# Kernel optimization log

Hardware: AMD Instinct MI355X
Metric: run time of the kernel (lower is better)

## Reference

```python
import jax, jax.numpy as jnp
import numpy as np

LAMBDA = 0.01  # sparsity_threshold
SCALE = 0.02
NUM_BLOCKS = 4


def setup_inputs() -> dict:
    key = jax.random.key(0)
    k1, k2, k3, k4, k5 = jax.random.split(key, 5)
    B, N, C = 8, 4096, 512
    bs = C // NUM_BLOCKS
    return {
        "x": jax.random.normal(k1, (B, N, C), dtype=jnp.float32),
        "w1": jax.random.normal(k2, (2, NUM_BLOCKS, bs, bs), dtype=jnp.float32) * SCALE,
        "w2": jax.random.normal(k3, (2, NUM_BLOCKS, bs, bs), dtype=jnp.float32) * SCALE,
        "b1": jax.random.normal(k4, (2, NUM_BLOCKS, bs), dtype=jnp.float32) * SCALE,
        "b2": jax.random.normal(k5, (2, NUM_BLOCKS, bs), dtype=jnp.float32) * SCALE,
        "H": 64,
        "W": 64,
    }


def _softshrink(v):
    return jnp.where(v > LAMBDA, v - LAMBDA, jnp.where(v < -LAMBDA, v + LAMBDA, jnp.zeros((), v.dtype)))


def reference(x, w1, w2, b1, b2, H, W):
    B, N, C = x.shape
    bs = C // NUM_BLOCKS
    xb = x.reshape(B, N, NUM_BLOCKS, bs)
    # FFT over (token, block) axes, ortho norm — faithful to torch fft2(dim=(1,2))
    xf = jnp.fft.fft2(xb, axes=(1, 2), norm="ortho")
    re, im = jnp.real(xf), jnp.imag(xf)

    mul = lambda a, w: jnp.einsum("tnbd,bdk->tnbk", a, w)  # block-diagonal matmul

    r1 = jax.nn.relu(mul(re, w1[0]) - mul(im, w1[1]) + b1[0])
    i1 = jax.nn.relu(mul(re, w1[1]) + mul(im, w1[0]) + b1[1])
    r2 = mul(r1, w2[0]) - mul(i1, w2[1]) + b2[0]
    i2 = mul(r1, w2[1]) + mul(i1, w2[0]) + b2[1]

    z = _softshrink(r2) + 1j * _softshrink(i2)
    out = jnp.real(jnp.fft.ifft2(z, axes=(1, 2), norm="ortho"))  # .to(float32) keeps real part
    return out.reshape(B, N, C).astype(jnp.float32)
```

## Files before the change

### kernel.cpp

```cpp
#include <hip/hip_runtime.h>
#include <math.h>

#define TWO_PI 6.283185307179586f

typedef __attribute__((ext_vector_type(8))) short bf16x8;
typedef __attribute__((ext_vector_type(4))) short bf16x4;
typedef __attribute__((ext_vector_type(4))) float f32x4;
typedef __attribute__((ext_vector_type(4))) _Float16 h16x4;
typedef __attribute__((ext_vector_type(8))) _Float16 h16x8;

__device__ __forceinline__ short f2bf(float f) {
    unsigned u = __float_as_uint(f);
    unsigned r = (u + 0x7FFFu + ((u >> 16) & 1u)) >> 16;
    return (short)r;
}
__device__ __forceinline__ float bf2f(short s) {
    return __uint_as_float(((unsigned)(unsigned short)s) << 16);
}

__device__ __forceinline__ int dr4(int s) {
    return ((s & 3) << 4) | (s & 12) | ((s >> 4) & 3);
}

__device__ __forceinline__ void cmulw(float& xr, float& xi, float wr, float wi) {
    const float tr = xr * wr - xi * wi;
    xi = xr * wi + xi * wr;
    xr = tr;
}

template<int W>
__device__ __forceinline__ void fft64_dif4v(_Float16 (*Lre)[W], _Float16 (*Lim)[W],
                                            const float* wtr, const float* wti,
                                            int c4, int h) {
#pragma unroll
    for (int s = 0; s < 3; ++s) {
        const int q  = 16 >> (2 * s);
        const int tw = 1 << (2 * s);
        __syncthreads();
        const int j = h & (q - 1);
        const int g = (s == 0) ? 0 : (h >> (4 - 2 * s));
        const int i0 = g * (q << 2) + j;
        const int i1 = i0 + q, i2 = i1 + q, i3 = i2 + q;
        const h16x4 A0r = *(const h16x4*)&Lre[i0][c4], A0i = *(const h16x4*)&Lim[i0][c4];
        const h16x4 A1r = *(const h16x4*)&Lre[i1][c4], A1i = *(const h16x4*)&Lim[i1][c4];
        const h16x4 A2r = *(const h16x4*)&Lre[i2][c4], A2i = *(const h16x4*)&Lim[i2][c4];
        const h16x4 A3r = *(const h16x4*)&Lre[i3][c4], A3i = *(const h16x4*)&Lim[i3][c4];
        const int m = j * tw;
        const float w1r = wtr[m],     w1i = wti[m];
        const float w2r = wtr[2 * m], w2i = wti[2 * m];
        const float w3r = wtr[3 * m], w3i = wti[3 * m];
        h16x4 O0r, O0i, O1r, O1i, O2r, O2i, O3r, O3i;
#pragma unroll
        for (int e = 0; e < 4; ++e) {
            const float a0r = (float)A0r[e], a0i = (float)A0i[e];
            const float a1r = (float)A1r[e], a1i = (float)A1i[e];
            const float a2r = (float)A2r[e], a2i = (float)A2i[e];
            const float a3r = (float)A3r[e], a3i = (float)A3i[e];
            const float t0r = a0r + a2r, t0i = a0i + a2i;
            const float t2r = a0r - a2r, t2i = a0i - a2i;
            const float t1r = a1r + a3r, t1i = a1i + a3i;
            const float dr  = a1r - a3r, di  = a1i - a3i;
            const float t3r = di, t3i = -dr;
            O0r[e] = (_Float16)(t0r + t1r);  O0i[e] = (_Float16)(t0i + t1i);
            float y1r = t2r + t3r, y1i = t2i + t3i;
            float y2r = t0r - t1r, y2i = t0i - t1i;
            float y3r = t2r - t3r, y3i = t2i - t3i;
            if (m) {
                cmulw(y1r, y1i, w1r, w1i);
                cmulw(y2r, y2i, w2r, w2i);
                cmulw(y3r, y3i, w3r, w3i);
            }
            O1r[e] = (_Float16)y1r; O1i[e] = (_Float16)y1i;
            O2r[e] = (_Float16)y2r; O2i[e] = (_Float16)y2i;
            O3r[e] = (_Float16)y3r; O3i[e] = (_Float16)y3i;
        }
        *(h16x4*)&Lre[i0][c4] = O0r;  *(h16x4*)&Lim[i0][c4] = O0i;
        *(h16x4*)&Lre[i1][c4] = O1r;  *(h16x4*)&Lim[i1][c4] = O1i;
        *(h16x4*)&Lre[i2][c4] = O2r;  *(h16x4*)&Lim[i2][c4] = O2i;
        *(h16x4*)&Lre[i3][c4] = O3r;  *(h16x4*)&Lim[i3][c4] = O3i;
    }
    __syncthreads();
}

template<int W>
__device__ __forceinline__ void fft64_dit4v(_Float16 (*Lre)[W], _Float16 (*Lim)[W],
                                            const float* wtr, const float* wti,
                                            int c4, int h) {
#pragma unroll
    for (int s = 2; s >= 0; --s) {
        const int q  = 16 >> (2 * s);
        const int tw = 1 << (2 * s);
        __syncthreads();
        const int j = h & (q - 1);
        const int g = (s == 0) ? 0 : (h >> (4 - 2 * s));
        const int i0 = g * (q << 2) + j;
        const int i1 = i0 + q, i2 = i1 + q, i3 = i2 + q;
        const h16x4 A0r = *(const h16x4*)&Lre[i0][c4], A0i = *(const h16x4*)&Lim[i0][c4];
        const h16x4 A1r = *(const h16x4*)&Lre[i1][c4], A1i = *(const h16x4*)&Lim[i1][c4];
        const h16x4 A2r = *(const h16x4*)&Lre[i2][c4], A2i = *(const h16x4*)&Lim[i2][c4];
        const h16x4 A3r = *(const h16x4*)&Lre[i3][c4], A3i = *(const h16x4*)&Lim[i3][c4];
        const int m = j * tw;
        const float w1r = wtr[m],     w1i = -wti[m];
        const float w2r = wtr[2 * m], w2i = -wti[2 * m];
        const float w3r = wtr[3 * m], w3i = -wti[3 * m];
        h16x4 O0r, O0i, O1r, O1i, O2r, O2i, O3r, O3i;
#pragma unroll
        for (int e = 0; e < 4; ++e) {
            float b1r = (float)A1r[e], b1i = (float)A1i[e];
            float b2r = (float)A2r[e], b2i = (float)A2i[e];
            float b3r = (float)A3r[e], b3i = (float)A3i[e];
            if (m) {
                cmulw(b1r, b1i, w1r, w1i);
                cmulw(b2r, b2i, w2r, w2i);
                cmulw(b3r, b3i, w3r, w3i);
            }
            const float a0r = (float)A0r[e], a0i = (float)A0i[e];
            const float u0r = a0r + b2r, u0i = a0i + b2i;
            const float u1r = a0r - b2r, u1i = a0i - b2i;
            const float u2r = b1r + b3r, u2i = b1i + b3i;
            const float dr  = b1r - b3r, di  = b1i - b3i;
            const float u3r = -di, u3i = dr;
            O0r[e] = (_Float16)(u0r + u2r); O0i[e] = (_Float16)(u0i + u2i);
            O1r[e] = (_Float16)(u1r + u3r); O1i[e] = (_Float16)(u1i + u3i);
            O2r[e] = (_Float16)(u0r - u2r); O2i[e] = (_Float16)(u0i - u2i);
            O3r[e] = (_Float16)(u1r - u3r); O3i[e] = (_Float16)(u1i - u3i);
        }
        *(h16x4*)&Lre[i0][c4] = O0r;  *(h16x4*)&Lim[i0][c4] = O0i;
        *(h16x4*)&Lre[i1][c4] = O1r;  *(h16x4*)&Lim[i1][c4] = O1i;
        *(h16x4*)&Lre[i2][c4] = O2r;  *(h16x4*)&Lim[i2][c4] = O2i;
        *(h16x4*)&Lre[i3][c4] = O3r;  *(h16x4*)&Lim[i3][c4] = O3i;
    }
    __syncthreads();
}

#define DECODE_BCT() \
    const int b  = blockIdx.x >> 8; \
    const int dg = (blockIdx.x >> 2) & 63; \
    const int ct = blockIdx.x & 3;

#define GADDR(slot, blk, f4) \
    (((size_t)(b * 4096 + (slot)) * 512) + (size_t)((blk) * 128 + ct * 32 + (f4) * 4))

#define GADDR8(slot, blk, e8) \
    (((size_t)(b * 4096 + (slot)) * 512) + (size_t)((blk) * 128 + ct * 32 + (e8) * 8))

#define SETUP_TABLE48() \
    if (tid < 48) { \
        float s_, c_; \
        sincosf(TWO_PI * (float)tid / 64.0f, &s_, &c_); \
        wre[tid] = c_; wim[tid] = -s_; \
    }

extern "C" __global__ void __launch_bounds__(512)
fft_fwd_a(const float* __restrict__ x, short* __restrict__ zre, short* __restrict__ zim) {
    __shared__ __align__(16) _Float16 Lre[64][136];
    __shared__ __align__(16) _Float16 Lim[64][136];
    __shared__ float wre[48], wim[48];
    __shared__ float twr[64], twi[64];
    const int tid = threadIdx.x;
    SETUP_TABLE48();
    DECODE_BCT();
    if (tid >= 64 && tid < 128) {
        const int s1 = tid - 64;
        float sn, cs;
        sincosf(-(TWO_PI / 4096.0f) * (float)(dg * dr4(s1)), &sn, &cs);
        twr[s1] = cs; twi[s1] = sn;
    }
    for (int idx = tid; idx < 2048; idx += 512) {
        const int n1 = idx >> 5, q = idx & 31, blk = q >> 3, f4 = q & 7;
        const int cl = blk * 32 + f4 * 4;
        const float4 v = *(const float4*)(x + GADDR(n1 * 64 + dg, blk, f4));
        h16x4 hv, hz;
        hv[0] = (_Float16)v.x; hv[1] = (_Float16)v.y;
        hv[2] = (_Float16)v.z; hv[3] = (_Float16)v.w;
        hz[0] = (_Float16)0.f; hz[1] = (_Float16)0.f;
        hz[2] = (_Float16)0.f; hz[3] = (_Float16)0.f;
        *(h16x4*)&Lre[n1][cl] = hv;
        *(h16x4*)&Lim[n1][cl] = hz;
    }
    fft64_dif4v<136>(Lre, Lim, wre, wim, (tid & 31) * 4, tid >> 5);
    {
        const int s1 = tid >> 3, f4 = tid & 7;
        const float cs = twr[s1], sn = twi[s1];
        f32x4 r[4], m[4];
#pragma unroll
        for (int blk = 0; blk < 4; ++blk) {
            const int cl = blk * 32 + f4 * 4;
            const h16x4 hr = *(const h16x4*)&Lre[s1][cl];
            const h16x4 hi = *(const h16x4*)&Lim[s1][cl];
#pragma unroll
            for (int e = 0; e < 4; ++e) {
                const float vr = (float)hr[e], vi = (float)hi[e];
                r[blk][e] = vr * cs - vi * sn;
                m[blk][e] = vr * sn + vi * cs;
            }
        }
        const float sc = 1.0f / 128.0f;
        f32x4 yr[4], ym[4];
#pragma unroll
        for (int e = 0; e < 4; ++e) {
            const float r0 = r[0][e], r1 = r[1][e], r2 = r[2][e], r3 = r[3][e];
            const float m0 = m[0][e], m1 = m[1][e], m2 = m[2][e], m3 = m[3][e];
            yr[0][e] = (r0 + r1 + r2 + r3) * sc;  ym[0][e] = (m0 + m1 + m2 + m3) * sc;
            yr[1][e] = (r0 + m1 - r2 - m3) * sc;  ym[1][e] = (m0 - r1 - m2 + r3) * sc;
            yr[2][e] = (r0 - r1 + r2 - r3) * sc;  ym[2][e] = (m0 - m1 + m2 - m3) * sc;
            yr[3][e] = (r0 - m1 - r2 + m3) * sc;  ym[3][e] = (m0 + r1 - m2 - r3) * sc;
        }
#pragma unroll
        for (int blk = 0; blk < 4; ++blk) {
            bf16x4 pr, pi;
#pragma unroll
            for (int e = 0; e < 4; ++e) {
                pr[e] = f2bf(yr[blk][e]);
                pi[e] = f2bf(ym[blk][e]);
            }
            const size_t g = GADDR(s1 * 64 + dg, blk, f4);
            *(bf16x4*)(zre + g) = pr;
            *(bf16x4*)(zim + g) = pi;
        }
    }
}

extern "C" __global__ void __launch_bounds__(512)
fft_fwd_b(short* __restrict__ zre, short* __restrict__ zim) {
    __shared__ __align__(16) _Float16 Lre[64][136];
    __shared__ __align__(16) _Float16 Lim[64][136];
    __shared__ float wre[48], wim[48];
    const int tid = threadIdx.x;
    SETUP_TABLE48();
    DECODE_BCT();
    for (int idx = tid; idx < 1024; idx += 512) {
        const int n2 = idx >> 4, q = idx & 15, blk = q >> 2, e8 = q & 3;
        const int cl = blk * 32 + e8 * 8;
        const size_t g = GADDR8(dg * 64 + n2, blk, e8);
        const bf16x8 vr = *(const bf16x8*)(zre + g);
        const bf16x8 vi = *(const bf16x8*)(zim + g);
        h16x8 hr, hi;
#pragma unroll
        for (int i = 0; i < 8; ++i) {
            hr[i] = (_Float16)bf2f(vr[i]);
            hi[i] = (_Float16)bf2f(vi[i]);
        }
        *(h16x8*)&Lre[n2][cl] = hr;
        *(h16x8*)&Lim[n2][cl] = hi;
    }
    fft64_dif4v<136>(Lre, Lim, wre, wim, (tid & 31) * 4, tid >> 5);
    for (int idx = tid; idx < 1024; idx += 512) {
        const int s2 = idx >> 4, q = idx & 15, blk = q >> 2, e8 = q & 3;
        const int cl = blk * 32 + e8 * 8;
        const h16x8 hr = *(const h16x8*)&Lre[s2][cl];
        const h16x8 hi = *(const h16x8*)&Lim[s2][cl];
        bf16x8 pr, pi;
#pragma unroll
        for (int i = 0; i < 8; ++i) {
            pr[i] = f2bf((float)hr[i]);
            pi[i] = f2bf((float)hi[i]);
        }
        const size_t g = GADDR8(dg * 64 + s2, blk, e8);
        *(bf16x8*)(zre + g) = pr;
        *(bf16x8*)(zim + g) = pi;
    }
}

extern "C" __global__ void __launch_bounds__(512)
fft_inv_a(short* __restrict__ zre, short* __restrict__ zim) {
    __shared__ __align__(16) _Float16 Lre[64][136];
    __shared__ __align__(16) _Float16 Lim[64][136];
    __shared__ float wre[48], wim[48];
    __shared__ float twr[64], twi[64];
    const int tid = threadIdx.x;
    SETUP_TABLE48();
    DECODE_BCT();
    if (tid >= 64 && tid < 128) {
        const int n2 = tid - 64;
        float sn, cs;
        sincosf((TWO_PI / 4096.0f) * (float)(n2 * dr4(dg)), &sn, &cs);
        twr[n2] = cs; twi[n2] = sn;
    }
    for (int idx = tid; idx < 1024; idx += 512) {
        const int s2 = idx >> 4, q = idx & 15, blk = q >> 2, e8 = q & 3;
        const int cl = blk * 32 + e8 * 8;
        const size_t g = GADDR8(dg * 64 + s2, blk, e8);
        const bf16x8 vr = *(const bf16x8*)(zre + g);
        const bf16x8 vi = *(const bf16x8*)(zim + g);
        h16x8 hr, hi;
#pragma unroll
        for (int i = 0; i < 8; ++i) {
            hr[i] = (_Float16)bf2f(vr[i]);
            hi[i] = (_Float16)bf2f(vi[i]);
        }
        *(h16x8*)&Lre[s2][cl] = hr;
        *(h16x8*)&Lim[s2][cl] = hi;
    }
    fft64_dit4v<136>(Lre, Lim, wre, wim, (tid & 31) * 4, tid >> 5);
    for (int idx = tid; idx < 2048; idx += 512) {
        const int n2 = idx >> 5, q = idx & 31, blk = q >> 3, f4 = q & 7;
        const int cl = blk * 32 + f4 * 4;
        const float cs = twr[n2], sn = twi[n2];
        const h16x4 hr = *(const h16x4*)&Lre[n2][cl];
        const h16x4 hi = *(const h16x4*)&Lim[n2][cl];
        bf16x4 pr, pi;
#pragma unroll
        for (int i = 0; i < 4; ++i) {
            const float vr = (float)hr[i], vi = (float)hi[i];
            pr[i] = f2bf(vr * cs - vi * sn);
            pi[i] = f2bf(vr * sn + vi * cs);
        }
        const size_t g = GADDR(dg * 64 + n2, blk, f4);
        *(bf16x4*)(zre + g) = pr;
        *(bf16x4*)(zim + g) = pi;
    }
}

extern "C" __global__ void __launch_bounds__(512)
fft_inv_b(const short* __restrict__ zre, const short* __restrict__ zim,
          float* __restrict__ out) {
    __shared__ __align__(16) _Float16 Lre[64][136];
    __shared__ __align__(16) _Float16 Lim[64][136];
    __shared__ float wre[48], wim[48];
    const int tid = threadIdx.x;
    SETUP_TABLE48();
    DECODE_BCT();
    {
        const int s1 = tid >> 3, f4 = tid & 7;
        f32x4 r[4], m[4];
#pragma unroll
        for (int blk = 0; blk < 4; ++blk) {
            const size_t g = GADDR(s1 * 64 + dg, blk, f4);
            const bf16x4 vr = *(const bf16x4*)(zre + g);
            const bf16x4 vi = *(const bf16x4*)(zim + g);
#pragma unroll
            for (int e = 0; e < 4; ++e) {
                r[blk][e] = bf2f(vr[e]);
                m[blk][e] = bf2f(vi[e]);
            }
        }
        const float sc = 1.0f / 128.0f;
        f32x4 yr[4], ym[4];
#pragma unroll
        for (int e = 0; e < 4; ++e) {
            const float r0 = r[0][e], r1 = r[1][e], r2 = r[2][e], r3 = r[3][e];
            const float m0 = m[0][e], m1 = m[1][e], m2 = m[2][e], m3 = m[3][e];
            yr[0][e] = (r0 + r1 + r2 + r3) * sc;  ym[0][e] = (m0 + m1 + m2 + m3) * sc;
            yr[1][e] = (r0 - m1 - r2 + m3) * sc;  ym[1][e] = (m0 + r1 - m2 - r3) * sc;
            yr[2][e] = (r0 - r1 + r2 - r3) * sc;  ym[2][e] = (m0 - m1 + m2 - m3) * sc;
            yr[3][e] = (r0 + m1 - r2 - m3) * sc;  ym[3][e] = (m0 - r1 - m2 + r3) * sc;
        }
#pragma unroll
        for (int blk = 0; blk < 4; ++blk) {
            const int cl = blk * 32 + f4 * 4;
            h16x4 hr, hi;
#pragma unroll
            for (int e = 0; e < 4; ++e) {
                hr[e] = (_Float16)yr[blk][e];
                hi[e] = (_Float16)ym[blk][e];
            }
            *(h16x4*)&Lre[s1][cl] = hr;
            *(h16x4*)&Lim[s1][cl] = hi;
        }
    }
    fft64_dit4v<136>(Lre, Lim, wre, wim, (tid & 31) * 4, tid >> 5);
    for (int idx = tid; idx < 2048; idx += 512) {
        const int n1 = idx >> 5, q = idx & 31, blk = q >> 3, f4 = q & 7;
        const int cl = blk * 32 + f4 * 4;
        const h16x4 hr = *(const h16x4*)&Lre[n1][cl];
        float4 o;
        o.x = (float)hr[0]; o.y = (float)hr[1];
        o.z = (float)hr[2]; o.w = (float)hr[3];
        *(float4*)(out + GADDR(n1 * 64 + dg, blk, f4)) = o;
    }
}

extern "C" __global__ void __launch_bounds__(256)
wprep(const float* __restrict__ w1, const float* __restrict__ w2,
      short* __restrict__ wb) {
    const int i4  = blockIdx.x * 256 + threadIdx.x;
    const int k0  = (i4 & 63) * 4;
    const int n   = (i4 >> 6) & 255;
    const int blk = (i4 >> 14) & 3;
    const int L   = i4 >> 16;
    const float* w = L ? w2 : w1;
    bf16x4 pv;
#pragma unroll
    for (int j = 0; j < 4; ++j) {
        const int k = k0 + j;
        float v;
        if (k < 128) {
            v = (n < 128) ? w[blk * 16384 + k * 128 + n]
                          : w[65536 + blk * 16384 + k * 128 + (n - 128)];
        } else {
            v = (n < 128) ? -w[65536 + blk * 16384 + (k - 128) * 128 + n]
                          :  w[blk * 16384 + (k - 128) * 128 + (n - 128)];
        }
        pv[j] = f2bf(v);
    }
    *(bf16x4*)(wb + (size_t)i4 * 4) = pv;
}

#define MITER 4

__device__ __forceinline__ void stage_tile(const short* __restrict__ zre,
                                           const short* __restrict__ zim,
                                           char* Abuf, int rowbase, int blk,
                                           int wave, int lane) {
#pragma unroll
    for (int it = 0; it < 4; ++it) {
        const int chunk = wave * 256 + it * 64 + lane;
        const int row   = chunk >> 5;
        const unsigned kbyte = ((unsigned)((chunk & 31) << 4)) ^ ((unsigned)((row & 7) << 4));
        const int k0 = (int)(kbyte >> 1);
        const short* src = (k0 < 128) ? zre : zim;
        const size_t g = (size_t)(rowbase + row) * 512 + blk * 128 + (k0 & 127);
        unsigned* lp = (unsigned*)(Abuf + (wave * 4096 + it * 1024));
        __builtin_amdgcn_global_load_lds((const unsigned*)(src + g), lp, 16, 0, 0);
    }
}

template<int LAYER>
__global__ void __launch_bounds__(512)
mlp_mfma(short* __restrict__ zre, short* __restrict__ zim,
         const short* __restrict__ wb, const float* __restrict__ bias) {
    __shared__ __align__(16) char As[2][64 * 256 * 2];

    const int blk  = blockIdx.y;
    const int tid  = threadIdx.x;
    const int wave = tid >> 6;
    const int lane = tid & 63;
    const int lrow = lane & 15;
    const int lk   = lane >> 4;

    bf16x8 Bf[2][8];
#pragma unroll
    for (int nt = 0; nt < 2; ++nt) {
        const int n = wave * 32 + nt * 16 + lrow;
#pragma unroll
        for (int ks = 0; ks < 8; ++ks) {
            Bf[nt][ks] = *(const bf16x8*)(wb + ((size_t)(blk * 256 + n) * 256 + ks * 32 + lk * 8));
        }
    }

    float bv[2];
#pragma unroll
    for (int nt = 0; nt < 2; ++nt) {
        const int n = wave * 32 + nt * 16 + lrow;
        bv[nt] = (n < 128) ? bias[blk * 128 + n] : bias[512 + blk * 128 + (n - 128)];
    }

    stage_tile(zre, zim, As[0], blockIdx.x * MITER * 64, blk, wave, lane);

    for (int t = 0; t < MITER; ++t) {
        __syncthreads();

        if (t + 1 < MITER)
            stage_tile(zre, zim, As[(t + 1) & 1],
                       (blockIdx.x * MITER + t + 1) * 64, blk, wave, lane);

        const char* Ab = As[t & 1];
        const int rowbase = (blockIdx.x * MITER + t) * 64;

        f32x4 acc[4][2];
#pragma unroll
        for (int mt = 0; mt < 4; ++mt)
#pragma unroll
            for (int nt = 0; nt < 2; ++nt)
                acc[mt][nt] = (f32x4){0.f, 0.f, 0.f, 0.f};

#pragma unroll
        for (int ks = 0; ks < 8; ++ks) {
            bf16x8 af[4];
#pragma unroll
            for (int mt = 0; mt < 4; ++mt) {
                const int row = mt * 16 + lrow;
                const int k0  = ks * 32 + lk * 8;
                const unsigned byteoff =
                    ((unsigned)(row * 512 + k0 * 2)) ^ ((unsigned)((row & 7) << 4));
                af[mt] = *(const bf16x8*)(Ab + byteoff);
            }
#pragma unroll
            for (int mt = 0; mt < 4; ++mt)
#pragma unroll
                for (int nt = 0; nt < 2; ++nt)
                    acc[mt][nt] = __builtin_amdgcn_mfma_f32_16x16x32_bf16(
                        af[mt], Bf[nt][ks], acc[mt][nt], 0, 0, 0);
        }

#pragma unroll
        for (int nt = 0; nt < 2; ++nt) {
            const int n = wave * 32 + nt * 16 + lrow;
            short* dst = (n < 128) ? zre : zim;
            const int col = blk * 128 + (n & 127);
#pragma unroll
            for (int mt = 0; mt < 4; ++mt) {
#pragma unroll
                for (int r = 0; r < 4; ++r) {
                    const int row = rowbase + mt * 16 + lk * 4 + r;
                    float v = acc[mt][nt][r] + bv[nt];
                    if (LAYER == 1) {
                        v = fmaxf(v, 0.0f);
                    } else {
                        v = (v > 0.01f) ? v - 0.01f : ((v < -0.01f) ? v + 0.01f : 0.0f);
                    }
                    dst[(size_t)row * 512 + col] = f2bf(v);
                }
            }
        }
    }
}

extern "C" void kernel_launch(void* const* d_in, const int* in_sizes, int n_in,
                              void* d_out, int out_size, void* d_ws, size_t ws_size,
                              hipStream_t stream) {
    const float* x  = (const float*)d_in[0];
    const float* w1 = (const float*)d_in[1];
    const float* w2 = (const float*)d_in[2];
    const float* b1 = (const float*)d_in[3];
    const float* b2 = (const float*)d_in[4];

    float* out = (float*)d_out;
    short* zre = (short*)d_ws;
    short* zim = zre + 16777216;
    short* wb  = (short*)d_out;
    const size_t WB_L = 4ull * 256 * 256;

    wprep<<<512, 256, 0, stream>>>(w1, w2, wb);

    fft_fwd_a<<<2048, 512, 0, stream>>>(x, zre, zim);
    fft_fwd_b<<<2048, 512, 0, stream>>>(zre, zim);

    mlp_mfma<1><<<dim3(32768 / (64 * MITER), 4), 512, 0, stream>>>(zre, zim, wb, b1);
    mlp_mfma<2><<<dim3(32768 / (64 * MITER), 4), 512, 0, stream>>>(zre, zim, wb + WB_L, b2);

    fft_inv_a<<<2048, 512, 0, stream>>>(zre, zim);
    fft_inv_b<<<2048, 512, 0, stream>>>(zre, zim, out);
}
```

Baseline: 219.0 us.

## Rewrite second FFT stage kernels with wavefront-shuffle radix-2 FFT and swizzled LDS

The fft_fwd_b and fft_inv_a kernels now load a 64-slot by 64-column window of bf16 data into an XOR-swizzled LDS tile. Each wavefront then does its 64-point FFT in registers with __shfl_xor butterflies, where the old code ran a radix-4 LDS FFT with a barrier per stage. The grid doubles to 4096 blocks, each covering half as many columns. The intent is to cut LDS traffic, barriers and fp16 conversions. In exchange there are more blocks, six shuffle stages of cross-lane work, and a change from DIF/DIT radix-4 ordering to radix-2, whose output ordering must still match the downstream kernels.

```diff
diff --git a/kernel.cpp b/kernel.cpp
--- a/kernel.cpp
+++ b/kernel.cpp
@@ -27,6 +27,21 @@
     xi = xr * wi + xi * wr;
     xr = tr;
 }
+
+#define DECODE_BCT() \
+    const int b  = blockIdx.x >> 8; \
+    const int dg = (blockIdx.x >> 2) & 63; \
+    const int ct = blockIdx.x & 3;
+
+#define GADDR(slot, blk, f4) \
+    (((size_t)(b * 4096 + (slot)) * 512) + (size_t)((blk) * 128 + ct * 32 + (f4) * 4))
+
+#define SETUP_TABLE48() \
+    if (tid < 48) { \
+        float s_, c_; \
+        sincosf(TWO_PI * (float)tid / 64.0f, &s_, &c_); \
+        wre[tid] = c_; wim[tid] = -s_; \
+    }
 
 template<int W>
 __device__ __forceinline__ void fft64_dif4v(_Float16 (*Lre)[W], _Float16 (*Lim)[W],
@@ -133,24 +148,6 @@
     __syncthreads();
 }
 
-#define DECODE_BCT() \
-    const int b  = blockIdx.x >> 8; \
-    const int dg = (blockIdx.x >> 2) & 63; \
-    const int ct = blockIdx.x & 3;
-
-#define GADDR(slot, blk, f4) \
-    (((size_t)(b * 4096 + (slot)) * 512) + (size_t)((blk) * 128 + ct * 32 + (f4) * 4))
-
-#define GADDR8(slot, blk, e8) \
-    (((size_t)(b * 4096 + (slot)) * 512) + (size_t)((blk) * 128 + ct * 32 + (e8) * 8))
-
-#define SETUP_TABLE48() \
-    if (tid < 48) { \
-        float s_, c_; \
-        sincosf(TWO_PI * (float)tid / 64.0f, &s_, &c_); \
-        wre[tid] = c_; wim[tid] = -s_; \
-    }
-
 extern "C" __global__ void __launch_bounds__(512)
 fft_fwd_a(const float* __restrict__ x, short* __restrict__ zre, short* __restrict__ zim) {
     __shared__ __align__(16) _Float16 Lre[64][136];
@@ -223,92 +220,148 @@
 
 extern "C" __global__ void __launch_bounds__(512)
 fft_fwd_b(short* __restrict__ zre, short* __restrict__ zim) {
-    __shared__ __align__(16) _Float16 Lre[64][136];
-    __shared__ __align__(16) _Float16 Lim[64][136];
+    __shared__ __align__(16) char Zs[16384];
     __shared__ float wre[48], wim[48];
     const int tid = threadIdx.x;
     SETUP_TABLE48();
-    DECODE_BCT();
-    for (int idx = tid; idx < 1024; idx += 512) {
-        const int n2 = idx >> 4, q = idx & 15, blk = q >> 2, e8 = q & 3;
-        const int cl = blk * 32 + e8 * 8;
-        const size_t g = GADDR8(dg * 64 + n2, blk, e8);
-        const bf16x8 vr = *(const bf16x8*)(zre + g);
-        const bf16x8 vi = *(const bf16x8*)(zim + g);
-        h16x8 hr, hi;
-#pragma unroll
-        for (int i = 0; i < 8; ++i) {
-            hr[i] = (_Float16)bf2f(vr[i]);
-            hi[i] = (_Float16)bf2f(vi[i]);
-        }
-        *(h16x8*)&Lre[n2][cl] = hr;
-        *(h16x8*)&Lim[n2][cl] = hi;
-    }
-    fft64_dif4v<136>(Lre, Lim, wre, wim, (tid & 31) * 4, tid >> 5);
-    for (int idx = tid; idx < 1024; idx += 512) {
-        const int s2 = idx >> 4, q = idx & 15, blk = q >> 2, e8 = q & 3;
-        const int cl = blk * 32 + e8 * 8;
-        const h16x8 hr = *(const h16x8*)&Lre[s2][cl];
-        const h16x8 hi = *(const h16x8*)&Lim[s2][cl];
-        bf16x8 pr, pi;
-#pragma unroll
-        for (int i = 0; i < 8; ++i) {
-            pr[i] = f2bf((float)hr[i]);
-            pi[i] = f2bf((float)hi[i]);
-        }
-        const size_t g = GADDR8(dg * 64 + s2, blk, e8);
-        *(bf16x8*)(zre + g) = pr;
-        *(bf16x8*)(zim + g) = pi;
+    const int b   = blockIdx.x >> 9;
+    const int dg  = (blockIdx.x >> 3) & 63;
+    const int win = blockIdx.x & 7;
+#pragma unroll
+    for (int k = 0; k < 2; ++k) {
+        const int idx = tid + k * 512;
+        const int p = idx >> 9;
+        const int r = idx & 511;
+        const int slot = r >> 3;
+        const int cj = r & 7;
+        const short* src = p ? zim : zre;
+        const bf16x8 v = *(const bf16x8*)(src + (size_t)(b * 4096 + dg * 64 + slot) * 512
+                                          + win * 64 + cj * 8);
+        *(bf16x8*)(Zs + p * 8192 + slot * 128 + ((cj * 16) ^ ((slot & 7) << 4))) = v;
+    }
+    __syncthreads();
+    const int lane = tid & 63, w = tid >> 6;
+    const int ro = lane * 128 + ((w * 16) ^ ((lane & 7) << 4));
+    {
+        const bf16x8 vr = *(const bf16x8*)(Zs + ro);
+        const bf16x8 vi = *(const bf16x8*)(Zs + 8192 + ro);
+        float cr[8], ci[8];
+#pragma unroll
+        for (int e = 0; e < 8; ++e) { cr[e] = bf2f(vr[e]); ci[e] = bf2f(vi[e]); }
+#pragma unroll
+        for (int t = 0; t < 6; ++t) {
+            const int span = 32 >> t;
+            const bool hi = (lane & span) != 0;
+            const int m = (lane & (span - 1)) << t;
+            const float wr_ = hi ? wre[m] : 1.0f;
+            const float wi_ = hi ? wim[m] : 0.0f;
+#pragma unroll
+            for (int e = 0; e < 8; ++e) {
+                const float pr = __shfl_xor(cr[e], span, 64);
+                const float pi = __shfl_xor(ci[e], span, 64);
+                const float sr = hi ? (pr - cr[e]) : (cr[e] + pr);
+                const float si = hi ? (pi - ci[e]) : (ci[e] + pi);
+                cr[e] = sr * wr_ - si * wi_;
+                ci[e] = sr * wi_ + si * wr_;
+            }
+        }
+        bf16x8 orr, oii;
+#pragma unroll
+        for (int e = 0; e < 8; ++e) { orr[e] = f2bf(cr[e]); oii[e] = f2bf(ci[e]); }
+        *(bf16x8*)(Zs + ro) = orr;
+        *(bf16x8*)(Zs + 8192 + ro) = oii;
+    }
+    __syncthreads();
+#pragma unroll
+    for (int k = 0; k < 2; ++k) {
+        const int idx = tid + k * 512;
+        const int p = idx >> 9;
+        const int r = idx & 511;
+        const int slot = r >> 3;
+        const int cj = r & 7;
+        const bf16x8 v = *(const bf16x8*)(Zs + p * 8192 + slot * 128 +
+                                          ((cj * 16) ^ ((slot & 7) << 4)));
+        short* dst = p ? zim : zre;
+        *(bf16x8*)(dst + (size_t)(b * 4096 + dg * 64 + slot) * 512 + win * 64 + cj * 8) = v;
     }
 }
 
 extern "C" __global__ void __launch_bounds__(512)
 fft_inv_a(short* __restrict__ zre, short* __restrict__ zim) {
-    __shared__ __align__(16) _Float16 Lre[64][136];
-    __shared__ __align__(16) _Float16 Lim[64][136];
+    __shared__ __align__(16) char Zs[16384];
     __shared__ float wre[48], wim[48];
     __shared__ float twr[64], twi[64];
     const int tid = threadIdx.x;
     SETUP_TABLE48();
-    DECODE_BCT();
+    const int b   = blockIdx.x >> 9;
+    const int dg  = (blockIdx.x >> 3) & 63;
+    const int win = blockIdx.x & 7;
     if (tid >= 64 && tid < 128) {
         const int n2 = tid - 64;
         float sn, cs;
         sincosf((TWO_PI / 4096.0f) * (float)(n2 * dr4(dg)), &sn, &cs);
         twr[n2] = cs; twi[n2] = sn;
     }
-    for (int idx = tid; idx < 1024; idx += 512) {
-        const int s2 = idx >> 4, q = idx & 15, blk = q >> 2, e8 = q & 3;
-        const int cl = blk * 32 + e8 * 8;
-        const size_t g = GADDR8(dg * 64 + s2, blk, e8);
-        const bf16x8 vr = *(const bf16x8*)(zre + g);
-        const bf16x8 vi = *(const bf16x8*)(zim + g);
-        h16x8 hr, hi;
-#pragma unroll
-        for (int i = 0; i < 8; ++i) {
-            hr[i] = (_Float16)bf2f(vr[i]);
-            hi[i] = (_Float16)bf2f(vi[i]);
-        }
-        *(h16x8*)&Lre[s2][cl] = hr;
-        *(h16x8*)&Lim[s2][cl] = hi;
-    }
-    fft64_dit4v<136>(Lre, Lim, wre, wim, (tid & 31) * 4, tid >> 5);
-    for (int idx = tid; idx < 2048; idx += 512) {
-        const int n2 = idx >> 5, q = idx & 31, blk = q >> 3, f4 = q & 7;
-        const int cl = blk * 32 + f4 * 4;
-        const float cs = twr[n2], sn = twi[n2];
-        const h16x4 hr = *(const h16x4*)&Lre[n2][cl];
-        const h16x4 hi = *(const h16x4*)&Lim[n2][cl];
-        bf16x4 pr, pi;
-#pragma unroll
-        for (int i = 0; i < 4; ++i) {
-            const float vr = (float)hr[i], vi = (float)hi[i];
-            pr[i] = f2bf(vr * cs - vi * sn);
-            pi[i] = f2bf(vr * sn + vi * cs);
-        }
-        const size_t g = GADDR(dg * 64 + n2, blk, f4);
-        *(bf16x4*)(zre + g) = pr;
-        *(bf16x4*)(zim + g) = pi;
+#pragma unroll
+    for (int k = 0; k < 2; ++k) {
+        const int idx = tid + k * 512;
+        const int p = idx >> 9;
+        const int r = idx & 511;
+        const int slot = r >> 3;
+        const int cj = r & 7;
+        const short* src = p ? zim : zre;
+        const bf16x8 v = *(const bf16x8*)(src + (size_t)(b * 4096 + dg * 64 + slot) * 512
+                                          + win * 64 + cj * 8);
+        *(bf16x8*)(Zs + p * 8192 + slot * 128 + ((cj * 16) ^ ((slot & 7) << 4))) = v;
+    }
+    __syncthreads();
+    const int lane = tid & 63, w = tid >> 6;
+    const int ro = lane * 128 + ((w * 16) ^ ((lane & 7) << 4));
+    {
+        const bf16x8 vr = *(const bf16x8*)(Zs + ro);
+        const bf16x8 vi = *(const bf16x8*)(Zs + 8192 + ro);
+        float cr[8], ci[8];
+#pragma unroll
+        for (int e = 0; e < 8; ++e) { cr[e] = bf2f(vr[e]); ci[e] = bf2f(vi[e]); }
+#pragma unroll
+        for (int t = 5; t >= 0; --t) {
+            const int span = 32 >> t;
+            const bool hi = (lane & span) != 0;
+            const int m = (lane & (span - 1)) << t;
+            const float wr_ = hi ? wre[m] : 1.0f;
+            const float wi_ = hi ? -wim[m] : 0.0f;
+#pragma unroll
+            for (int e = 0; e < 8; ++e) {
+                const float vr_ = cr[e] * wr_ - ci[e] * wi_;
+                const float vi_ = cr[e] * wi_ + ci[e] * wr_;
+                const float pr = __shfl_xor(vr_, span, 64);
+                const float pi = __shfl_xor(vi_, span, 64);
+                cr[e] = hi ? (pr - vr_) : (vr_ + pr);
+                ci[e] = hi ? (pi - vi_) : (vi_ + pi);
+            }
+        }
+        const float cs = twr[lane], sn = twi[lane];
+        bf16x8 orr, oii;
+#pragma unroll
+        for (int e = 0; e < 8; ++e) {
+            orr[e] = f2bf(cr[e] * cs - ci[e] * sn);
+            oii[e] = f2bf(cr[e] * sn + ci[e] * cs);
+        }
+        *(bf16x8*)(Zs + ro) = orr;
+        *(bf16x8*)(Zs + 8192 + ro) = oii;
+    }
+    __syncthreads();
+#pragma unroll
+    for (int k = 0; k < 2; ++k) {
+        const int idx = tid + k * 512;
+        const int p = idx >> 9;
+        const int r = idx & 511;
+        const int slot = r >> 3;
+        const int cj = r & 7;
+        const bf16x8 v = *(const bf16x8*)(Zs + p * 8192 + slot * 128 +
+                                          ((cj * 16) ^ ((slot & 7) << 4)));
+        short* dst = p ? zim : zre;
+        *(bf16x8*)(dst + (size_t)(b * 4096 + dg * 64 + slot) * 512 + win * 64 + cj * 8) = v;
     }
 }
 
@@ -525,11 +578,11 @@
     wprep<<<512, 256, 0, stream>>>(w1, w2, wb);
 
     fft_fwd_a<<<2048, 512, 0, stream>>>(x, zre, zim);
-    fft_fwd_b<<<2048, 512, 0, stream>>>(zre, zim);
+    fft_fwd_b<<<4096, 512, 0, stream>>>(zre, zim);
 
     mlp_mfma<1><<<dim3(32768 / (64 * MITER), 4), 512, 0, stream>>>(zre, zim, wb, b1);
     mlp_mfma<2><<<dim3(32768 / (64 * MITER), 4), 512, 0, stream>>>(zre, zim, wb + WB_L, b2);
 
-    fft_inv_a<<<2048, 512, 0, stream>>>(zre, zim);
+    fft_inv_a<<<4096, 512, 0, stream>>>(zre, zim);
     fft_inv_b<<<2048, 512, 0, stream>>>(zre, zim, out);
 }
```

Result: slower. 228.5 us (+4.3%).
